# Performance work log

Measured on AMD Instinct MI355X. Metric: run time of the kernel, lower is better.

## Reference

```python
import jax, jax.numpy as jnp
import numpy as np

B, T, I, H, L, C = 64, 256, 256, 512, 3, 1000  # seq_len T must equal input_size I per module's fc sizing


def setup_inputs() -> dict:
    key = jax.random.key(0)
    ks = jax.random.split(key, 20)
    s = 1.0 / np.sqrt(H)  # PyTorch LSTM init scale
    inp = {"x": jax.random.normal(ks[0], (B, T, I), dtype=jnp.float32)}
    k = 1
    for layer in range(L):
        in_dim = I if layer == 0 else H
        inp[f"W_ih{layer}"] = jax.random.uniform(ks[k], (4 * H, in_dim), minval=-s, maxval=s); k += 1
        inp[f"W_hh{layer}"] = jax.random.uniform(ks[k], (4 * H, H), minval=-s, maxval=s); k += 1
        inp[f"b_ih{layer}"] = jax.random.uniform(ks[k], (4 * H,), minval=-s, maxval=s); k += 1
        inp[f"b_hh{layer}"] = jax.random.uniform(ks[k], (4 * H,), minval=-s, maxval=s); k += 1
    sf = 1.0 / np.sqrt(I * H)
    inp["fc_w"] = jax.random.uniform(ks[k], (C, I * H), minval=-sf, maxval=sf); k += 1
    inp["fc_b"] = jax.random.uniform(ks[k], (C,), minval=-sf, maxval=sf)
    return inp


def _lstm_layer(x, W_ih, W_hh, b_ih, b_hh):
    # x: [B, T, in_dim] -> [B, T, H]; PyTorch gate order: i, f, g, o
    b, t, _ = x.shape
    h_dim = W_hh.shape[1]
    xg = jnp.einsum('bti,gi->btg', x, W_ih) + b_ih + b_hh  # [B, T, 4H]
    xg = jnp.swapaxes(xg, 0, 1)  # [T, B, 4H]

    def step(carry, g_t):
        h, c = carry
        gates = g_t + h @ W_hh.T
        i, f, g, o = jnp.split(gates, 4, axis=-1)
        c = jax.nn.sigmoid(f) * c + jax.nn.sigmoid(i) * jnp.tanh(g)
        h = jax.nn.sigmoid(o) * jnp.tanh(c)
        return (h, c), h

    h0 = jnp.zeros((b, h_dim), x.dtype)
    _, hs = jax.lax.scan(step, (h0, h0), xg)
    return jnp.swapaxes(hs, 0, 1)  # [B, T, H]


def reference(x, W_ih0, W_hh0, b_ih0, b_hh0, W_ih1, W_hh1, b_ih1, b_hh1,
              W_ih2, W_hh2, b_ih2, b_hh2, fc_w, fc_b):
    # 3-layer unidirectional LSTM (inference: inter-layer dropout is identity)
    y = _lstm_layer(x, W_ih0, W_hh0, b_ih0, b_hh0)
    y = _lstm_layer(y, W_ih1, W_hh1, b_ih1, b_hh1)
    y = _lstm_layer(y, W_ih2, W_hh2, b_ih2, b_hh2)
    flat = y.reshape(y.shape[0], -1)  # [B, T*H]
    return flat @ fc_w.T + fc_b  # [B, C]
```

## Files before the change

### kernel.cpp

```cpp
#include <hip/hip_runtime.h>
#include <hip/hip_bf16.h>

#define Bb 64
#define Tt 256
#define Ii 256
#define Hh 512
#define Cc 1000
#define SENT 0x7F80u

typedef float f4 __attribute__((ext_vector_type(4)));
typedef short s8 __attribute__((ext_vector_type(8)));
typedef unsigned long long u64;

__device__ __forceinline__ unsigned short f2bf(float f) {
  union { float f; unsigned u; } v; v.f = f;
  return (unsigned short)((v.u + 0x7FFFu + ((v.u >> 16) & 1u)) >> 16);
}
__device__ __forceinline__ float sigf(float x) {
  return __builtin_amdgcn_rcpf(1.f + __expf(-x));
}
__device__ __forceinline__ float tanhs(float x) {
  float ax = fabsf(x);
  float e = __expf(-2.f * ax);
  float r = (1.f - e) * __builtin_amdgcn_rcpf(1.f + e);
  return copysignf(r, x);
}

__device__ __forceinline__ s8 ld128_llc(const unsigned short* p) {
  s8 v;
  asm volatile("global_load_dwordx4 %0, %1, off sc0 sc1" : "=&v"(v) : "v"(p) : "memory");
  return v;
}
#define VMCNT0 asm volatile("s_waitcnt vmcnt(0)" ::: "memory")
#define SBAR __builtin_amdgcn_sched_barrier(0)

__device__ __forceinline__ bool chk(s8 v) {
  return ((unsigned short)v[0] != (unsigned short)SENT) &
         ((unsigned short)v[4] != (unsigned short)SENT);
}

struct PT {
  const float* x;
  const float* Whh[3]; const float* Wih[3];
  const float* bih[3]; const float* bhh[3];
  const float* fcw;
  float* outbuf;
  unsigned short* y[3];
  unsigned* fl;
  unsigned* fcfl;
};

__global__ void zero_sync(unsigned* f) {
  int i = blockIdx.x * 256 + threadIdx.x;
  if (i < 8192) f[i] = 0;
}

__global__ void fill_y(u64* p) {
  const u64 pat = 0x7F807F807F807F80ull;
  size_t g = (size_t)blockIdx.x * 256 + threadIdx.x;
#pragma unroll
  for (int i = 0; i < 16; ++i)
    __hip_atomic_store(p + g + (size_t)i * 393216, pat, __ATOMIC_RELAXED,
                       __HIP_MEMORY_SCOPE_AGENT);
}

__global__ void bias_init_kernel(const float* __restrict__ fcb, float* __restrict__ out) {
  int i = blockIdx.x * 256 + threadIdx.x;
  if (i < Bb * Cc) out[i] = fcb[i % Cc];
}

__launch_bounds__(256, 1)
__global__ void mega_kernel(PT p) {
  const int bid = blockIdx.x;
  const int tid = threadIdx.x;
  const int lane = tid & 63;
  const int w = tid >> 6;
  const int q = lane >> 4;
  const int c = lane & 15;
  const int b = 16 * w + c;

  __shared__ unsigned short Whl[64 * 512];
  __shared__ unsigned short Wil[64 * 512];

  if (bid < 96) {
    const int L = bid >> 5;
    const int s = bid & 31;
    const int n0 = s * 16;

    const int Kin = (L == 0) ? Ii : Hh;
    {
      const float* src = p.Whh[L];
      for (int idx = tid; idx < 64 * 64; idx += 256) {
        int r = idx >> 6, kk = (idx & 63) << 3;
        int rho = r & 15, tt = r >> 4;
        int j = (rho & 3) * Hh + n0 + 4 * (rho >> 2) + tt;
        const float* sr = src + (size_t)j * Hh + kk;
        s8 tv;
#pragma unroll
        for (int e = 0; e < 8; ++e) tv[e] = (short)f2bf(sr[e]);
        int byt = ((r * 512 + kk) * 2) ^ ((r & 7) << 4);
        *(s8*)((char*)Whl + byt) = tv;
      }
      const float* si = p.Wih[L];
      const int kd8 = Kin >> 3;
      for (int idx = tid; idx < 64 * kd8; idx += 256) {
        int r = idx / kd8, kk = (idx - r * kd8) << 3;
        int rho = r & 15, tt = r >> 4;
        int j = (rho & 3) * Hh + n0 + 4 * (rho >> 2) + tt;
        const float* sr = si + (size_t)j * Kin + kk;
        s8 tv;
#pragma unroll
        for (int e = 0; e < 8; ++e) tv[e] = (short)f2bf(sr[e]);
        int byt = ((r * Kin + kk) * 2) ^ ((r & 7) << 4);
        *(s8*)((char*)Wil + byt) = tv;
      }
    }

    f4 bias[4];
#pragma unroll
    for (int tt = 0; tt < 4; ++tt)
#pragma unroll
      for (int g = 0; g < 4; ++g) {
        int bi = g * Hh + n0 + 4 * q + tt;
        bias[tt][g] = p.bih[L][bi] + p.bhh[L][bi];
      }
    float cst[4] = {0.f, 0.f, 0.f, 0.f};
    __syncthreads();

    const int aswz = (c & 7) << 4;
    unsigned short* yl = p.y[L];
    const unsigned short* ylow = (L > 0) ? p.y[L - 1] : (const unsigned short*)0;
    unsigned* flin = (L > 0) ? p.fl + ((L - 1) * 32) * 4 * 16 : (unsigned*)0;
    unsigned* flown = p.fl + (L * 32) * 4 * 16;
    unsigned* myfl = p.fl + ((L * 32 + s) * 4 + w) * 16;

    for (int t = 0; t < Tt; ++t) {
      f4 acc[4];
#pragma unroll
      for (int tt = 0; tt < 4; ++tt) acc[tt] = bias[tt];

      if (L == 0) {
        const float* xr = p.x + ((size_t)b * Tt + t) * Ii + 8 * q;
#pragma unroll
        for (int kc = 0; kc < 8; ++kc) {
          f4 xa = *(const f4*)(xr + kc * 32);
          f4 xc = *(const f4*)(xr + kc * 32 + 4);
          s8 xb;
#pragma unroll
          for (int e = 0; e < 4; ++e) { xb[e] = (short)f2bf(xa[e]); xb[e + 4] = (short)f2bf(xc[e]); }
#pragma unroll
          for (int tt = 0; tt < 4; ++tt) {
            int byt = (((tt * 16 + c) * 256 + kc * 32 + 8 * q) * 2) ^ aswz;
            s8 wa = *(const s8*)((const char*)Wil + byt);
            acc[tt] = __builtin_amdgcn_mfma_f32_16x16x32_bf16(wa, xb, acc[tt], 0, 0, 0);
          }
        }
      } else {
        const unsigned short* yr = ylow + ((size_t)b * Tt + t) * Hh + 8 * q;
        s8 yb[16];
#pragma unroll
        for (int kc = 0; kc < 16; ++kc) yb[kc] = ld128_llc(yr + kc * 32);
        while (!__all(lane < 32
                          ? __hip_atomic_load(flin + (lane * 4 + w) * 16, __ATOMIC_RELAXED,
                                              __HIP_MEMORY_SCOPE_AGENT) >= (unsigned)(t + 1)
                          : true))
          __builtin_amdgcn_s_sleep(1);
        asm volatile("" ::: "memory");
        VMCNT0; SBAR;
        while (1) {
          unsigned bad = 0;
#pragma unroll
          for (int kc = 0; kc < 16; ++kc)
            if (!chk(yb[kc])) bad |= (1u << kc);
          if (__all(bad == 0)) break;
          __builtin_amdgcn_s_sleep(1);
#pragma unroll
          for (int kc = 0; kc < 16; ++kc)
            if (bad & (1u << kc)) yb[kc] = ld128_llc(yr + kc * 32);
          VMCNT0; SBAR;
        }
#pragma unroll
        for (int tt = 0; tt < 4; ++tt)
#pragma unroll
          for (int kc = 0; kc < 16; ++kc) {
            int byt = (((tt * 16 + c) * 512 + kc * 32 + 8 * q) * 2) ^ aswz;
            s8 wa = *(const s8*)((const char*)Wil + byt);
            acc[tt] = __builtin_amdgcn_mfma_f32_16x16x32_bf16(wa, yb[kc], acc[tt], 0, 0, 0);
          }
      }

      if (t > 0) {
        const unsigned short* hr = yl + ((size_t)b * Tt + (t - 1)) * Hh + 8 * q;
        s8 hb[16];
#pragma unroll
        for (int kc = 0; kc < 16; ++kc) hb[kc] = ld128_llc(hr + kc * 32);
        while (!__all(lane < 32
                          ? __hip_atomic_load(flown + (lane * 4 + w) * 16, __ATOMIC_RELAXED,
                                              __HIP_MEMORY_SCOPE_AGENT) >= (unsigned)t
                          : true))
          __builtin_amdgcn_s_sleep(1);
        asm volatile("" ::: "memory");
        VMCNT0; SBAR;
        while (1) {
          unsigned bad = 0;
#pragma unroll
          for (int kc = 0; kc < 16; ++kc)
            if (!chk(hb[kc])) bad |= (1u << kc);
          if (__all(bad == 0)) break;
          __builtin_amdgcn_s_sleep(1);
#pragma unroll
          for (int kc = 0; kc < 16; ++kc)
            if (bad & (1u << kc)) hb[kc] = ld128_llc(hr + kc * 32);
          VMCNT0; SBAR;
        }
#pragma unroll
        for (int tt = 0; tt < 4; ++tt)
#pragma unroll
          for (int kc = 0; kc < 16; ++kc) {
            int byt = (((tt * 16 + c) * 512 + kc * 32 + 8 * q) * 2) ^ aswz;
            s8 wa = *(const s8*)((const char*)Whl + byt);
            acc[tt] = __builtin_amdgcn_mfma_f32_16x16x32_bf16(wa, hb[kc], acc[tt], 0, 0, 0);
          }
      }

      unsigned short hu[4];
#pragma unroll
      for (int tt = 0; tt < 4; ++tt) {
        float ii = sigf(acc[tt][0]), ff = sigf(acc[tt][1]);
        float gg = tanhs(acc[tt][2]), oo = sigf(acc[tt][3]);
        cst[tt] = ff * cst[tt] + ii * gg;
        hu[tt] = f2bf(oo * tanhs(cst[tt]));
      }
      u64 hv = (u64)hu[0] | ((u64)hu[1] << 16) | ((u64)hu[2] << 32) | ((u64)hu[3] << 48);
      u64* dst = (u64*)(yl + ((size_t)b * Tt + t) * Hh + n0 + 4 * q);
      __hip_atomic_store(dst, hv, __ATOMIC_RELAXED, __HIP_MEMORY_SCOPE_AGENT);
      if (lane == 0)
        __hip_atomic_store(myfl, (unsigned)(t + 1), __ATOMIC_RELAXED, __HIP_MEMORY_SCOPE_AGENT);
      if (L == 2 && (t & 7) == 7) {
        VMCNT0;
        if (lane == 0)
          __hip_atomic_store(p.fcfl + (s * 4 + w) * 16, (unsigned)(t + 1), __ATOMIC_RELAXED,
                             __HIP_MEMORY_SCOPE_AGENT);
      }
    }
  } else {
    const int fcid = bid - 96;
    const int KT = Tt * Hh;
    const unsigned short* y2 = p.y[2];
    for (int ti = fcid; ti < 1024; ti += 160) {
      const int kch = ti >> 5, ct = ti & 31;
      const unsigned tneed1 = (unsigned)(kch * 8 + 8);
      bool ok;
      do {
        unsigned v = 0xFFFFFFFFu;
        if (lane < 32) {
          unsigned mn = 0xFFFFFFFFu;
#pragma unroll
          for (int ww = 0; ww < 4; ++ww) {
            unsigned vv = __hip_atomic_load(p.fcfl + (lane * 4 + ww) * 16, __ATOMIC_RELAXED,
                                            __HIP_MEMORY_SCOPE_AGENT);
            mn = mn < vv ? mn : vv;
          }
          v = mn;
        }
        ok = __all(v >= tneed1);
        if (!ok) __builtin_amdgcn_s_sleep(16);
      } while (!ok);
      asm volatile("" ::: "memory");

      const int kbase = kch * 4096 + q * 8;
      const int c0 = ct * 32 + c;
      const int c1 = c0 + 16;
      const bool v0 = (c0 < Cc), v1 = (c1 < Cc);
      const float* w0 = p.fcw + (size_t)c0 * KT;
      const float* w1 = p.fcw + (size_t)c1 * KT;
      const unsigned short* yr = y2 + (size_t)b * KT;
      f4 a0 = {0.f, 0.f, 0.f, 0.f}, a1 = {0.f, 0.f, 0.f, 0.f};
      for (int kk = 0; kk < 4096; kk += 32) {
        const int k = kbase + kk;
        s8 bf = *(const s8*)(yr + k);
        s8 wa0 = {0, 0, 0, 0, 0, 0, 0, 0}, wa1 = {0, 0, 0, 0, 0, 0, 0, 0};
        if (v0) {
#pragma unroll
          for (int qq = 0; qq < 8; ++qq) wa0[qq] = (short)f2bf(w0[k + qq]);
        }
        if (v1) {
#pragma unroll
          for (int qq = 0; qq < 8; ++qq) wa1[qq] = (short)f2bf(w1[k + qq]);
        }
        a0 = __builtin_amdgcn_mfma_f32_16x16x32_bf16(wa0, bf, a0, 0, 0, 0);
        a1 = __builtin_amdgcn_mfma_f32_16x16x32_bf16(wa1, bf, a1, 0, 0, 0);
      }
      const int rr = q * 4;
#pragma unroll
      for (int qq = 0; qq < 4; ++qq) {
        int ca = ct * 32 + rr + qq;
        if (ca < Cc) atomicAdd(p.outbuf + (size_t)b * Cc + ca, a0[qq]);
        int cb2 = ca + 16;
        if (cb2 < Cc) atomicAdd(p.outbuf + (size_t)b * Cc + cb2, a1[qq]);
      }
    }
  }
}

extern "C" void kernel_launch(void* const* d_in, const int* in_sizes, int n_in,
                              void* d_out, int out_size, void* d_ws, size_t ws_size,
                              hipStream_t stream) {
  PT p;
  p.x = (const float*)d_in[0];
  p.Wih[0] = (const float*)d_in[1];  p.Whh[0] = (const float*)d_in[2];
  p.bih[0] = (const float*)d_in[3];  p.bhh[0] = (const float*)d_in[4];
  p.Wih[1] = (const float*)d_in[5];  p.Whh[1] = (const float*)d_in[6];
  p.bih[1] = (const float*)d_in[7];  p.bhh[1] = (const float*)d_in[8];
  p.Wih[2] = (const float*)d_in[9];  p.Whh[2] = (const float*)d_in[10];
  p.bih[2] = (const float*)d_in[11]; p.bhh[2] = (const float*)d_in[12];
  p.fcw = (const float*)d_in[13];
  const float* fcb = (const float*)d_in[14];
  p.outbuf = (float*)d_out;

  char* ws = (char*)d_ws;
  p.fl = (unsigned*)ws;
  p.fcfl = p.fl + 6144;
  const size_t ysz = (size_t)Bb * Tt * Hh;
  unsigned short* y0 = (unsigned short*)(ws + 65536);
  p.y[0] = y0;
  p.y[1] = y0 + ysz;
  p.y[2] = y0 + 2 * ysz;

  zero_sync<<<32, 256, 0, stream>>>(p.fl);
  fill_y<<<1536, 256, 0, stream>>>((u64*)y0);
  bias_init_kernel<<<250, 256, 0, stream>>>(fcb, (float*)d_out);
  mega_kernel<<<256, 256, 0, stream>>>(p);
}
```

Baseline: 1.753 ms.

## Drop per-step flag polling and rely on sentinel checks per k-chunk

Removes the per-wave progress flags for the recurrent layers. Consumers no longer spin on counters before reading h/y; they check each 128-bit chunk for the sentinel value and start the MFMAs on a chunk once it is valid, so readiness checks interleave with compute. This cuts the flag-store and flag-poll round trips on the serial timestep chain. In exchange, correctness now depends on the sentinel bits being visible only after the data, with no flag ordering. Retries are also per chunk with sleeps, which may stall the MFMA stream.

After: 2.336 ms. +33.3%, slower.

```diff
diff --git a/kernel.cpp b/kernel.cpp
--- a/kernel.cpp
+++ b/kernel.cpp
@@ -46,13 +46,12 @@
   const float* fcw;
   float* outbuf;
   unsigned short* y[3];
-  unsigned* fl;
   unsigned* fcfl;
 };
 
 __global__ void zero_sync(unsigned* f) {
   int i = blockIdx.x * 256 + threadIdx.x;
-  if (i < 8192) f[i] = 0;
+  if (i < 2048) f[i] = 0;
 }
 
 __global__ void fill_y(u64* p) {
@@ -130,9 +129,6 @@
     const int aswz = (c & 7) << 4;
     unsigned short* yl = p.y[L];
     const unsigned short* ylow = (L > 0) ? p.y[L - 1] : (const unsigned short*)0;
-    unsigned* flin = (L > 0) ? p.fl + ((L - 1) * 32) * 4 * 16 : (unsigned*)0;
-    unsigned* flown = p.fl + (L * 32) * 4 * 16;
-    unsigned* myfl = p.fl + ((L * 32 + s) * 4 + w) * 16;
 
     for (int t = 0; t < Tt; ++t) {
       f4 acc[4];
@@ -160,33 +156,21 @@
         s8 yb[16];
 #pragma unroll
         for (int kc = 0; kc < 16; ++kc) yb[kc] = ld128_llc(yr + kc * 32);
-        while (!__all(lane < 32
-                          ? __hip_atomic_load(flin + (lane * 4 + w) * 16, __ATOMIC_RELAXED,
-                                              __HIP_MEMORY_SCOPE_AGENT) >= (unsigned)(t + 1)
-                          : true))
-          __builtin_amdgcn_s_sleep(1);
-        asm volatile("" ::: "memory");
         VMCNT0; SBAR;
-        while (1) {
-          unsigned bad = 0;
-#pragma unroll
-          for (int kc = 0; kc < 16; ++kc)
-            if (!chk(yb[kc])) bad |= (1u << kc);
-          if (__all(bad == 0)) break;
-          __builtin_amdgcn_s_sleep(1);
-#pragma unroll
-          for (int kc = 0; kc < 16; ++kc)
-            if (bad & (1u << kc)) yb[kc] = ld128_llc(yr + kc * 32);
-          VMCNT0; SBAR;
-        }
-#pragma unroll
-        for (int tt = 0; tt < 4; ++tt)
-#pragma unroll
-          for (int kc = 0; kc < 16; ++kc) {
+#pragma unroll
+        for (int kc = 0; kc < 16; ++kc) {
+          while (!__all(chk(yb[kc]))) {
+            __builtin_amdgcn_s_sleep(1);
+            yb[kc] = ld128_llc(yr + kc * 32);
+            VMCNT0; SBAR;
+          }
+#pragma unroll
+          for (int tt = 0; tt < 4; ++tt) {
             int byt = (((tt * 16 + c) * 512 + kc * 32 + 8 * q) * 2) ^ aswz;
             s8 wa = *(const s8*)((const char*)Wil + byt);
             acc[tt] = __builtin_amdgcn_mfma_f32_16x16x32_bf16(wa, yb[kc], acc[tt], 0, 0, 0);
           }
+        }
       }
 
       if (t > 0) {
@@ -194,33 +178,21 @@
         s8 hb[16];
 #pragma unroll
         for (int kc = 0; kc < 16; ++kc) hb[kc] = ld128_llc(hr + kc * 32);
-        while (!__all(lane < 32
-                          ? __hip_atomic_load(flown + (lane * 4 + w) * 16, __ATOMIC_RELAXED,
-                                              __HIP_MEMORY_SCOPE_AGENT) >= (unsigned)t
-                          : true))
-          __builtin_amdgcn_s_sleep(1);
-        asm volatile("" ::: "memory");
         VMCNT0; SBAR;
-        while (1) {
-          unsigned bad = 0;
-#pragma unroll
-          for (int kc = 0; kc < 16; ++kc)
-            if (!chk(hb[kc])) bad |= (1u << kc);
-          if (__all(bad == 0)) break;
-          __builtin_amdgcn_s_sleep(1);
-#pragma unroll
-          for (int kc = 0; kc < 16; ++kc)
-            if (bad & (1u << kc)) hb[kc] = ld128_llc(hr + kc * 32);
-          VMCNT0; SBAR;
-        }
-#pragma unroll
-        for (int tt = 0; tt < 4; ++tt)
-#pragma unroll
-          for (int kc = 0; kc < 16; ++kc) {
+#pragma unroll
+        for (int kc = 0; kc < 16; ++kc) {
+          while (!__all(chk(hb[kc]))) {
+            __builtin_amdgcn_s_sleep(1);
+            hb[kc] = ld128_llc(hr + kc * 32);
+            VMCNT0; SBAR;
+          }
+#pragma unroll
+          for (int tt = 0; tt < 4; ++tt) {
             int byt = (((tt * 16 + c) * 512 + kc * 32 + 8 * q) * 2) ^ aswz;
             s8 wa = *(const s8*)((const char*)Whl + byt);
             acc[tt] = __builtin_amdgcn_mfma_f32_16x16x32_bf16(wa, hb[kc], acc[tt], 0, 0, 0);
           }
+        }
       }
 
       unsigned short hu[4];
@@ -234,8 +206,6 @@
       u64 hv = (u64)hu[0] | ((u64)hu[1] << 16) | ((u64)hu[2] << 32) | ((u64)hu[3] << 48);
       u64* dst = (u64*)(yl + ((size_t)b * Tt + t) * Hh + n0 + 4 * q);
       __hip_atomic_store(dst, hv, __ATOMIC_RELAXED, __HIP_MEMORY_SCOPE_AGENT);
-      if (lane == 0)
-        __hip_atomic_store(myfl, (unsigned)(t + 1), __ATOMIC_RELAXED, __HIP_MEMORY_SCOPE_AGENT);
       if (L == 2 && (t & 7) == 7) {
         VMCNT0;
         if (lane == 0)
@@ -319,15 +289,14 @@
   p.outbuf = (float*)d_out;
 
   char* ws = (char*)d_ws;
-  p.fl = (unsigned*)ws;
-  p.fcfl = p.fl + 6144;
+  p.fcfl = (unsigned*)ws;
   const size_t ysz = (size_t)Bb * Tt * Hh;
   unsigned short* y0 = (unsigned short*)(ws + 65536);
   p.y[0] = y0;
   p.y[1] = y0 + ysz;
   p.y[2] = y0 + 2 * ysz;
 
-  zero_sync<<<32, 256, 0, stream>>>(p.fl);
+  zero_sync<<<8, 256, 0, stream>>>(p.fcfl);
   fill_y<<<1536, 256, 0, stream>>>((u64*)y0);
   bias_init_kernel<<<250, 256, 0, stream>>>(fcb, (float*)d_out);
   mega_kernel<<<256, 256, 0, stream>>>(p);
```

## Software-pipeline input projection of next timestep after publishing hidden state

Applied to the files above, without the earlier changes.

The input-to-hidden MFMA contribution for step t+1 is now computed right after h_t is stored and its flag published, instead of at the start of step t+1. This moves the input GEMM off the recurrent critical path, so it overlaps with waiting for other blocks' h_t. The h loads are also moved after the flag wait rather than issued speculatively before it. The cost is a peeled prologue and duplicated code.

Measured after the change: 1.761 ms. Within noise of the previous version (+0.5%).

```diff
diff --git a/kernel.cpp b/kernel.cpp
--- a/kernel.cpp
+++ b/kernel.cpp
@@ -134,72 +134,72 @@
     unsigned* flown = p.fl + (L * 32) * 4 * 16;
     unsigned* myfl = p.fl + ((L * 32 + s) * 4 + w) * 16;
 
+    f4 acc[4];
+
+#pragma unroll
+    for (int tt = 0; tt < 4; ++tt) acc[tt] = bias[tt];
+    if (L == 0) {
+      const float* xr = p.x + ((size_t)b * Tt + 0) * Ii + 8 * q;
+#pragma unroll
+      for (int kc = 0; kc < 8; ++kc) {
+        f4 xa = *(const f4*)(xr + kc * 32);
+        f4 xc = *(const f4*)(xr + kc * 32 + 4);
+        s8 xb;
+#pragma unroll
+        for (int e = 0; e < 4; ++e) { xb[e] = (short)f2bf(xa[e]); xb[e + 4] = (short)f2bf(xc[e]); }
+#pragma unroll
+        for (int tt = 0; tt < 4; ++tt) {
+          int byt = (((tt * 16 + c) * 256 + kc * 32 + 8 * q) * 2) ^ aswz;
+          s8 wa = *(const s8*)((const char*)Wil + byt);
+          acc[tt] = __builtin_amdgcn_mfma_f32_16x16x32_bf16(wa, xb, acc[tt], 0, 0, 0);
+        }
+      }
+    } else {
+      while (!__all(lane < 32
+                        ? __hip_atomic_load(flin + (lane * 4 + w) * 16, __ATOMIC_RELAXED,
+                                            __HIP_MEMORY_SCOPE_AGENT) >= 1u
+                        : true))
+        __builtin_amdgcn_s_sleep(1);
+      asm volatile("" ::: "memory");
+      const unsigned short* yr = ylow + ((size_t)b * Tt + 0) * Hh + 8 * q;
+      s8 yb[16];
+#pragma unroll
+      for (int kc = 0; kc < 16; ++kc) yb[kc] = ld128_llc(yr + kc * 32);
+      VMCNT0; SBAR;
+      while (1) {
+        unsigned bad = 0;
+#pragma unroll
+        for (int kc = 0; kc < 16; ++kc)
+          if (!chk(yb[kc])) bad |= (1u << kc);
+        if (__all(bad == 0)) break;
+        __builtin_amdgcn_s_sleep(1);
+#pragma unroll
+        for (int kc = 0; kc < 16; ++kc)
+          if (bad & (1u << kc)) yb[kc] = ld128_llc(yr + kc * 32);
+        VMCNT0; SBAR;
+      }
+#pragma unroll
+      for (int tt = 0; tt < 4; ++tt)
+#pragma unroll
+        for (int kc = 0; kc < 16; ++kc) {
+          int byt = (((tt * 16 + c) * 512 + kc * 32 + 8 * q) * 2) ^ aswz;
+          s8 wa = *(const s8*)((const char*)Wil + byt);
+          acc[tt] = __builtin_amdgcn_mfma_f32_16x16x32_bf16(wa, yb[kc], acc[tt], 0, 0, 0);
+        }
+    }
+
     for (int t = 0; t < Tt; ++t) {
-      f4 acc[4];
-#pragma unroll
-      for (int tt = 0; tt < 4; ++tt) acc[tt] = bias[tt];
-
-      if (L == 0) {
-        const float* xr = p.x + ((size_t)b * Tt + t) * Ii + 8 * q;
-#pragma unroll
-        for (int kc = 0; kc < 8; ++kc) {
-          f4 xa = *(const f4*)(xr + kc * 32);
-          f4 xc = *(const f4*)(xr + kc * 32 + 4);
-          s8 xb;
-#pragma unroll
-          for (int e = 0; e < 4; ++e) { xb[e] = (short)f2bf(xa[e]); xb[e + 4] = (short)f2bf(xc[e]); }
-#pragma unroll
-          for (int tt = 0; tt < 4; ++tt) {
-            int byt = (((tt * 16 + c) * 256 + kc * 32 + 8 * q) * 2) ^ aswz;
-            s8 wa = *(const s8*)((const char*)Wil + byt);
-            acc[tt] = __builtin_amdgcn_mfma_f32_16x16x32_bf16(wa, xb, acc[tt], 0, 0, 0);
-          }
-        }
-      } else {
-        const unsigned short* yr = ylow + ((size_t)b * Tt + t) * Hh + 8 * q;
-        s8 yb[16];
-#pragma unroll
-        for (int kc = 0; kc < 16; ++kc) yb[kc] = ld128_llc(yr + kc * 32);
-        while (!__all(lane < 32
-                          ? __hip_atomic_load(flin + (lane * 4 + w) * 16, __ATOMIC_RELAXED,
-                                              __HIP_MEMORY_SCOPE_AGENT) >= (unsigned)(t + 1)
-                          : true))
-          __builtin_amdgcn_s_sleep(1);
-        asm volatile("" ::: "memory");
-        VMCNT0; SBAR;
-        while (1) {
-          unsigned bad = 0;
-#pragma unroll
-          for (int kc = 0; kc < 16; ++kc)
-            if (!chk(yb[kc])) bad |= (1u << kc);
-          if (__all(bad == 0)) break;
-          __builtin_amdgcn_s_sleep(1);
-#pragma unroll
-          for (int kc = 0; kc < 16; ++kc)
-            if (bad & (1u << kc)) yb[kc] = ld128_llc(yr + kc * 32);
-          VMCNT0; SBAR;
-        }
-#pragma unroll
-        for (int tt = 0; tt < 4; ++tt)
-#pragma unroll
-          for (int kc = 0; kc < 16; ++kc) {
-            int byt = (((tt * 16 + c) * 512 + kc * 32 + 8 * q) * 2) ^ aswz;
-            s8 wa = *(const s8*)((const char*)Wil + byt);
-            acc[tt] = __builtin_amdgcn_mfma_f32_16x16x32_bf16(wa, yb[kc], acc[tt], 0, 0, 0);
-          }
-      }
-
       if (t > 0) {
         const unsigned short* hr = yl + ((size_t)b * Tt + (t - 1)) * Hh + 8 * q;
         s8 hb[16];
-#pragma unroll
-        for (int kc = 0; kc < 16; ++kc) hb[kc] = ld128_llc(hr + kc * 32);
         while (!__all(lane < 32
                           ? __hip_atomic_load(flown + (lane * 4 + w) * 16, __ATOMIC_RELAXED,
                                               __HIP_MEMORY_SCOPE_AGENT) >= (unsigned)t
                           : true))
           __builtin_amdgcn_s_sleep(1);
         asm volatile("" ::: "memory");
+#pragma unroll
+        for (int kc = 0; kc < 16; ++kc) hb[kc] = ld128_llc(hr + kc * 32);
         VMCNT0; SBAR;
         while (1) {
           unsigned bad = 0;
@@ -241,6 +241,60 @@
         if (lane == 0)
           __hip_atomic_store(p.fcfl + (s * 4 + w) * 16, (unsigned)(t + 1), __ATOMIC_RELAXED,
                              __HIP_MEMORY_SCOPE_AGENT);
+      }
+
+      if (t + 1 < Tt) {
+#pragma unroll
+        for (int tt = 0; tt < 4; ++tt) acc[tt] = bias[tt];
+        if (L == 0) {
+          const float* xr = p.x + ((size_t)b * Tt + (t + 1)) * Ii + 8 * q;
+#pragma unroll
+          for (int kc = 0; kc < 8; ++kc) {
+            f4 xa = *(const f4*)(xr + kc * 32);
+            f4 xc = *(const f4*)(xr + kc * 32 + 4);
+            s8 xb;
+#pragma unroll
+            for (int e = 0; e < 4; ++e) { xb[e] = (short)f2bf(xa[e]); xb[e + 4] = (short)f2bf(xc[e]); }
+#pragma unroll
+            for (int tt = 0; tt < 4; ++tt) {
+              int byt = (((tt * 16 + c) * 256 + kc * 32 + 8 * q) * 2) ^ aswz;
+              s8 wa = *(const s8*)((const char*)Wil + byt);
+              acc[tt] = __builtin_amdgcn_mfma_f32_16x16x32_bf16(wa, xb, acc[tt], 0, 0, 0);
+            }
+          }
+        } else {
+          while (!__all(lane < 32
+                            ? __hip_atomic_load(flin + (lane * 4 + w) * 16, __ATOMIC_RELAXED,
+                                                __HIP_MEMORY_SCOPE_AGENT) >= (unsigned)(t + 2)
+                            : true))
+            __builtin_amdgcn_s_sleep(1);
+          asm volatile("" ::: "memory");
+          const unsigned short* yr = ylow + ((size_t)b * Tt + (t + 1)) * Hh + 8 * q;
+          s8 yb[16];
+#pragma unroll
+          for (int kc = 0; kc < 16; ++kc) yb[kc] = ld128_llc(yr + kc * 32);
+          VMCNT0; SBAR;
+          while (1) {
+            unsigned bad = 0;
+#pragma unroll
+            for (int kc = 0; kc < 16; ++kc)
+              if (!chk(yb[kc])) bad |= (1u << kc);
+            if (__all(bad == 0)) break;
+            __builtin_amdgcn_s_sleep(1);
+#pragma unroll
+            for (int kc = 0; kc < 16; ++kc)
+              if (bad & (1u << kc)) yb[kc] = ld128_llc(yr + kc * 32);
+            VMCNT0; SBAR;
+          }
+#pragma unroll
+          for (int tt = 0; tt < 4; ++tt)
+#pragma unroll
+            for (int kc = 0; kc < 16; ++kc) {
+              int byt = (((tt * 16 + c) * 512 + kc * 32 + 8 * q) * 2) ^ aswz;
+              s8 wa = *(const s8*)((const char*)Wil + byt);
+              acc[tt] = __builtin_amdgcn_mfma_f32_16x16x32_bf16(wa, yb[kc], acc[tt], 0, 0, 0);
+            }
+        }
       }
     }
   } else {
```
